# Performance work log

Measured on AMD Instinct MI355X. Metric: run time of the kernel, lower is better.

## Reference

```python
import jax, jax.numpy as jnp
import numpy as np

B, DIM, HEADS, HD, H, W = 1, 256, 8, 32, 64, 64
MLP = int(DIM * 4.0)
EPS = 1e-5


def _ln(x, g, b):
    # LayerNorm over channel dim of NCHW (torch applies it on NHWC last dim)
    mu = x.mean(axis=1, keepdims=True)
    var = ((x - mu) ** 2).mean(axis=1, keepdims=True)
    return (x - mu) / jnp.sqrt(var + EPS) * g[None, :, None, None] + b[None, :, None, None]


def _c1(x, w, b):
    # 1x1 conv: w is [out, in]
    return jnp.einsum('bchw,oc->bohw', x, w) + b[None, :, None, None]


def _c3(x, w, b):
    y = jax.lax.conv_general_dilated(x, w, (1, 1), ((1, 1), (1, 1)),
                                     dimension_numbers=('NCHW', 'OIHW', 'NCHW'))
    return y + b[None, :, None, None]


def setup_inputs() -> dict:
    key = jax.random.key(0)
    ks = jax.random.split(key, 16)
    init = lambda k, s: jax.random.normal(k, s, jnp.float32) * 0.02
    d = {}
    d['rgb_feat'] = jax.random.normal(ks[0], (B, DIM, H, W), jnp.float32)
    d['dpt_feat'] = jax.random.normal(ks[1], (B, DIM, H, W), jnp.float32)
    d['x_dpt'] = jax.random.normal(ks[2], (B, 1, 1024, 1024), jnp.float32)
    d['wq'] = init(ks[3], (DIM, DIM)); d['bq'] = jnp.zeros((DIM,), jnp.float32)
    d['wk'] = init(ks[4], (DIM, DIM)); d['bk'] = jnp.zeros((DIM,), jnp.float32)
    d['wv'] = init(ks[5], (DIM, DIM)); d['bv'] = jnp.zeros((DIM,), jnp.float32)
    d['wo'] = init(ks[6], (DIM, DIM)); d['bo'] = jnp.zeros((DIM,), jnp.float32)
    d['g_rgb'] = jnp.ones((DIM,), jnp.float32); d['b_rgb'] = jnp.zeros((DIM,), jnp.float32)
    d['g_dpt'] = jnp.ones((DIM,), jnp.float32); d['b_dpt'] = jnp.zeros((DIM,), jnp.float32)
    d['g1'] = jnp.ones((DIM,), jnp.float32); d['b1'] = jnp.zeros((DIM,), jnp.float32)
    d['g2'] = jnp.ones((DIM,), jnp.float32); d['b2'] = jnp.zeros((DIM,), jnp.float32)
    d['w_mlp1'] = init(ks[7], (MLP, DIM)); d['b_mlp1'] = jnp.zeros((MLP,), jnp.float32)
    d['w_mlp2'] = init(ks[8], (DIM, MLP)); d['b_mlp2'] = jnp.zeros((DIM,), jnp.float32)
    d['w_de1'] = init(ks[9], (DIM, 1, 3, 3)); d['b_de1'] = jnp.zeros((DIM,), jnp.float32)
    d['w_de2'] = init(ks[10], (DIM, DIM)); d['b_de2'] = jnp.zeros((DIM,), jnp.float32)
    d['pos_emb'] = init(ks[11], (1, DIM, 1, 1))
    d['scale'] = jnp.sqrt(jnp.float32(HD))
    return d


def reference(rgb_feat, dpt_feat, x_dpt, wq, bq, wk, bk, wv, bv, wo, bo,
              g_rgb, b_rgb, g_dpt, b_dpt, g1, b1, g2, b2,
              w_mlp1, b_mlp1, w_mlp2, b_mlp2, w_de1, b_de1, w_de2, b_de2,
              pos_emb, scale):
    Bn, C, Hh, Ww = rgb_feat.shape
    n = Hh * Ww
    rgb_ln = _ln(rgb_feat, g_rgb, b_rgb)
    dpt_ln = _ln(dpt_feat, g_dpt, b_dpt)
    # depth positional embedding: bilinear downsample (align_corners=False) + conv3x3 + relu + conv1x1
    xd = jax.image.resize(x_dpt, (Bn, 1, Hh, Ww), method='bilinear', antialias=False)
    pe = _c1(jax.nn.relu(_c3(xd, w_de1, b_de1)), w_de2, b_de2)
    rgb_ln = rgb_ln + pos_emb + pe
    dpt_ln = dpt_ln + pos_emb + pe
    # QKV as [B, heads, head_dim, N]
    q = _c1(rgb_ln, wq, bq).reshape(Bn, HEADS, HD, n)
    k = _c1(dpt_ln, wk, bk).reshape(Bn, HEADS, HD, n)
    v = _c1(dpt_ln, wv, bv).reshape(Bn, HEADS, HD, n)
    scores = jnp.einsum('bhdn,bhdm->bhnm', q, k) / scale
    attn = jax.nn.softmax(scores, axis=-1)  # dropout is identity in eval
    fused = jnp.einsum('bhnm,bhdm->bhdn', attn, v).reshape(Bn, C, Hh, Ww)
    out = _c1(fused, wo, bo) + rgb_feat
    out_ln = _ln(out, g1, b1)
    h = jax.nn.gelu(_c1(out_ln, w_mlp1, b_mlp1), approximate=False)
    mlp_out = _c1(h, w_mlp2, b_mlp2)
    out2 = mlp_out + out_ln
    return _ln(out2, g2, b2)
```

## Files before the change

### kernel.cpp

```cpp
#include <hip/hip_runtime.h>
#include <hip/hip_bf16.h>
#include <math.h>

constexpr int NTOK = 4096;
constexpr int CDIM = 256;
constexpr int MLPD = 1024;
constexpr int SPLIT = 4;
constexpr float EPS_LN = 1e-5f;

typedef __attribute__((ext_vector_type(8))) short bf16x8;
typedef __attribute__((ext_vector_type(4))) float floatx4;
typedef __attribute__((ext_vector_type(16))) float f32x16;
typedef unsigned short u16;
typedef unsigned int u32;

__device__ __forceinline__ u16 f2bf(float x) {
    union { float f; u32 u; } v; v.f = x;
    u32 r = v.u + 0x7fff + ((v.u >> 16) & 1);
    return (u16)(r >> 16);
}
__device__ __forceinline__ float bf2f(u16 u) {
    union { u32 i; float f; } v; v.i = ((u32)u) << 16; return v.f;
}
__device__ __forceinline__ u32 pkbf(float a, float b) {
    __hip_bfloat162 h = __float22bfloat162_rn(make_float2(a, b));
    union { __hip_bfloat162 h; u32 u; } v; v.h = h; return v.u;
}
__device__ __forceinline__ float gelu_exact(float x) {
    return 0.5f * x * (1.0f + erff(x * 0.70710678118654752f));
}

__global__ __launch_bounds__(256) void k_prep(const float* __restrict__ rgb,
                                              float* __restrict__ rgbT,
                                              const float* __restrict__ dpt,
                                              float* __restrict__ dptT,
                                              const float* __restrict__ xdpt,
                                              const float* __restrict__ w3,
                                              const float* __restrict__ b3,
                                              u16* __restrict__ y,
                                              const float* __restrict__ wq,
                                              const float* __restrict__ wk,
                                              const float* __restrict__ wv,
                                              const float* __restrict__ wo,
                                              const float* __restrict__ wde2,
                                              const float* __restrict__ wm1,
                                              const float* __restrict__ wm2,
                                              u16* __restrict__ arena) {
    int blk = blockIdx.x;
    int t = threadIdx.x;
    if (blk < 512) {
        const float* in = (blk < 256) ? rgb : dpt;
        float* out = (blk < 256) ? rgbT : dptT;
        int tb = blk & 255;
        int c0 = (tb & 63) * 64, r0 = (tb >> 6) * 64;
        __shared__ float T[64][65];
        int rr = t >> 4, cc = (t & 15) * 4;
#pragma unroll
        for (int i = 0; i < 4; ++i) {
            int row = i * 16 + rr;
            float4 v = *(const float4*)(in + (size_t)(r0 + row) * NTOK + c0 + cc);
            T[row][cc] = v.x; T[row][cc + 1] = v.y; T[row][cc + 2] = v.z; T[row][cc + 3] = v.w;
        }
        __syncthreads();
#pragma unroll
        for (int i = 0; i < 4; ++i) {
            int a = i * 16 + rr;
            float4 v;
            v.x = T[cc][a]; v.y = T[cc + 1][a]; v.z = T[cc + 2][a]; v.w = T[cc + 3][a];
            *(float4*)(out + (size_t)(c0 + a) * CDIM + r0 + cc) = v;
        }
    } else if (blk < 768) {
        __shared__ float nb[3][18];
        int n0 = (blk - 512) * 16;
        int yy = n0 >> 6, x0 = n0 & 63;
        if (t < 54) {
            int r = t / 18, cc = t % 18;
            int sy = yy - 1 + r, sx = x0 - 1 + cc;
            float v = 0.f;
            if (sy >= 0 && sy < 64 && sx >= 0 && sx < 64) {
                int r0 = 16 * sy + 7, c0 = 16 * sx + 7;
                v = 0.25f * (xdpt[r0 * 1024 + c0] + xdpt[r0 * 1024 + c0 + 1] +
                             xdpt[(r0 + 1) * 1024 + c0] + xdpt[(r0 + 1) * 1024 + c0 + 1]);
            }
            nb[r][cc] = v;
        }
        __syncthreads();
        float wv9[9];
#pragma unroll
        for (int i = 0; i < 9; ++i) wv9[i] = w3[t * 9 + i];
        float bb = b3[t];
#pragma unroll
        for (int k = 0; k < 16; ++k) {
            float acc = bb;
#pragma unroll
            for (int r = 0; r < 3; ++r)
#pragma unroll
                for (int kx = 0; kx < 3; ++kx) acc += wv9[r * 3 + kx] * nb[r][k + kx];
            y[(size_t)(n0 + k) * CDIM + t] = f2bf(fmaxf(acc, 0.f));
        }
    } else {
        int e0 = (blk - 768) * 1024 + t * 4;
        const float* src; int off;
        if (e0 < 65536)       { src = wq;   off = 0; }
        else if (e0 < 131072) { src = wk;   off = 65536; }
        else if (e0 < 196608) { src = wv;   off = 131072; }
        else if (e0 < 262144) { src = wo;   off = 196608; }
        else if (e0 < 327680) { src = wde2; off = 262144; }
        else if (e0 < 589824) { src = wm1;  off = 327680; }
        else                  { src = wm2;  off = 589824; }
        float4 v = *(const float4*)(src + (e0 - off));
        uint2 o; o.x = pkbf(v.x, v.y); o.y = pkbf(v.z, v.w);
        *(uint2*)(arena + e0) = o;
    }
}

__global__ __launch_bounds__(256) void k_lnT(const void* __restrict__ xA,
                                             const float* __restrict__ gA,
                                             const float* __restrict__ bA,
                                             void* __restrict__ yA,
                                             const void* __restrict__ xB,
                                             const float* __restrict__ gB,
                                             const float* __restrict__ bB,
                                             void* __restrict__ yB,
                                             const u16* __restrict__ pe,
                                             const float* __restrict__ pos,
                                             int xf32) {
    const void* x; const float* g; const float* bb; void* y;
    if (blockIdx.y == 0) { x = xA; g = gA; bb = bA; y = yA; }
    else                 { x = xB; g = gB; bb = bB; y = yB; }
    int n = blockIdx.x * 4 + (threadIdx.x >> 6);
    int lane = threadIdx.x & 63;
    int c = lane * 4;
    float4 xv;
    if (xf32) {
        xv = *((const float4*)x + (size_t)n * 64 + lane);
    } else {
        ushort4 u = *((const ushort4*)x + (size_t)n * 64 + lane);
        xv = make_float4(bf2f(u.x), bf2f(u.y), bf2f(u.z), bf2f(u.w));
    }
    float s = xv.x + xv.y + xv.z + xv.w;
    float s2 = xv.x * xv.x + xv.y * xv.y + xv.z * xv.z + xv.w * xv.w;
#pragma unroll
    for (int off = 1; off < 64; off <<= 1) {
        s += __shfl_xor(s, off, 64);
        s2 += __shfl_xor(s2, off, 64);
    }
    float mu = s * (1.0f / 256.0f);
    float var = s2 * (1.0f / 256.0f) - mu * mu;
    float rsd = rsqrtf(var + EPS_LN);
    float4 g4 = *(const float4*)(g + c);
    float4 b4 = *(const float4*)(bb + c);
    float4 o;
    o.x = (xv.x - mu) * rsd * g4.x + b4.x;
    o.y = (xv.y - mu) * rsd * g4.y + b4.y;
    o.z = (xv.z - mu) * rsd * g4.z + b4.z;
    o.w = (xv.w - mu) * rsd * g4.w + b4.w;
    if (pe) {
        float4 p4 = *(const float4*)(pos + c);
        ushort4 pu = *((const ushort4*)pe + (size_t)n * 64 + lane);
        o.x += p4.x + bf2f(pu.x);
        o.y += p4.y + bf2f(pu.y);
        o.z += p4.z + bf2f(pu.z);
        o.w += p4.w + bf2f(pu.w);
    }
    ushort4 ou;
    ou.x = f2bf(o.x); ou.y = f2bf(o.y); ou.z = f2bf(o.z); ou.w = f2bf(o.w);
    *((ushort4*)y + (size_t)n * 64 + lane) = ou;
}

#define LDB 72
__global__ __launch_bounds__(512) void k_bmm(const u16* __restrict__ X0, const void* __restrict__ W0,
                                             const float* __restrict__ B0, void* __restrict__ Y0, int f0,
                                             const u16* __restrict__ X1, const void* __restrict__ W1,
                                             const float* __restrict__ B1, void* __restrict__ Y1, int f1,
                                             const u16* __restrict__ X2, const void* __restrict__ W2,
                                             const float* __restrict__ B2, void* __restrict__ Y2, int f2,
                                             const void* __restrict__ res, const float* __restrict__ scl,
                                             int M, int K) {
    const u16* X; const void* Wp; const float* bias; void* Yp; int flags;
    if (blockIdx.z == 0)      { X = X0; Wp = W0; bias = B0; Yp = Y0; flags = f0; }
    else if (blockIdx.z == 1) { X = X1; Wp = W1; bias = B1; Yp = Y1; flags = f1; }
    else                      { X = X2; Wp = W2; bias = B2; Yp = Y2; flags = f2; }
    __shared__ u16 Xs[2][64 * LDB];
    __shared__ u16 Ws[2][64 * LDB];
    float* Cred = (float*)&Xs[0][0];

    int tid = threadIdx.x;
    int kg = tid >> 8;
    int t = tid & 255;
    int wid = t >> 6, lane = t & 63;
    int lo16 = lane & 15, quad = lane >> 4;
    int wy = wid & 1, wx = wid >> 1;
    int n0 = blockIdx.x * 64, m0 = blockIdx.y * 64;
    int srow = t >> 2, sseg = t & 3;
    int Khalf = K >> 1;
    int kbase = kg * Khalf;

    floatx4 acc[2][2];
#pragma unroll
    for (int i = 0; i < 2; ++i)
#pragma unroll
        for (int j = 0; j < 2; ++j) acc[i][j] = floatx4{0.f, 0.f, 0.f, 0.f};

    for (int k0 = 0; k0 < Khalf; k0 += 64) {
        int kk = kbase + k0;
        const u16* xp = X + (size_t)(n0 + srow) * K + kk + sseg * 16;
        uint4 xr0 = *(const uint4*)xp;
        uint4 xr1 = *(const uint4*)(xp + 8);
        uint4 wb0, wb1;
        if (flags & 32) {
            const u16* wp = (const u16*)Wp + (size_t)(m0 + srow) * K + kk + sseg * 16;
            wb0 = *(const uint4*)wp;
            wb1 = *(const uint4*)(wp + 8);
        } else {
            const float* wp = (const float*)Wp + (size_t)(m0 + srow) * K + kk + sseg * 16;
            float4 w0 = *(const float4*)wp;
            float4 w1 = *(const float4*)(wp + 4);
            float4 w2 = *(const float4*)(wp + 8);
            float4 w3 = *(const float4*)(wp + 12);
            wb0.x = pkbf(w0.x, w0.y); wb0.y = pkbf(w0.z, w0.w);
            wb0.z = pkbf(w1.x, w1.y); wb0.w = pkbf(w1.z, w1.w);
            wb1.x = pkbf(w2.x, w2.y); wb1.y = pkbf(w2.z, w2.w);
            wb1.z = pkbf(w3.x, w3.y); wb1.w = pkbf(w3.z, w3.w);
        }
        __syncthreads();
        *(uint4*)&Xs[kg][srow * LDB + sseg * 16] = xr0;
        *(uint4*)&Xs[kg][srow * LDB + sseg * 16 + 8] = xr1;
        *(uint4*)&Ws[kg][srow * LDB + sseg * 16] = wb0;
        *(uint4*)&Ws[kg][srow * LDB + sseg * 16 + 8] = wb1;
        __syncthreads();

        const u16* As = (flags & 2) ? &Ws[kg][0] : &Xs[kg][0];
        const u16* Bs = (flags & 2) ? &Xs[kg][0] : &Ws[kg][0];
#pragma unroll
        for (int h = 0; h < 2; ++h) {
            int ko = h * 32 + quad * 8;
            bf16x8 a0 = *(const bf16x8*)&As[(wy * 32 + lo16) * LDB + ko];
            bf16x8 a1 = *(const bf16x8*)&As[(wy * 32 + 16 + lo16) * LDB + ko];
            bf16x8 b0 = *(const bf16x8*)&Bs[(wx * 32 + lo16) * LDB + ko];
            bf16x8 b1 = *(const bf16x8*)&Bs[(wx * 32 + 16 + lo16) * LDB + ko];
            acc[0][0] = __builtin_amdgcn_mfma_f32_16x16x32_bf16(a0, b0, acc[0][0], 0, 0, 0);
            acc[0][1] = __builtin_amdgcn_mfma_f32_16x16x32_bf16(a0, b1, acc[0][1], 0, 0, 0);
            acc[1][0] = __builtin_amdgcn_mfma_f32_16x16x32_bf16(a1, b0, acc[1][0], 0, 0, 0);
            acc[1][1] = __builtin_amdgcn_mfma_f32_16x16x32_bf16(a1, b1, acc[1][1], 0, 0, 0);
        }
    }

    __syncthreads();
    if (kg == 1) {
        float* c = &Cred[t * 17];
#pragma unroll
        for (int i = 0; i < 2; ++i)
#pragma unroll
            for (int j = 0; j < 2; ++j)
#pragma unroll
                for (int r = 0; r < 4; ++r) c[(i * 2 + j) * 4 + r] = acc[i][j][r];
    }
    __syncthreads();
    if (kg == 1) return;
    {
        const float* c = &Cred[t * 17];
#pragma unroll
        for (int i = 0; i < 2; ++i)
#pragma unroll
            for (int j = 0; j < 2; ++j)
#pragma unroll
                for (int r = 0; r < 4; ++r) acc[i][j][r] += c[(i * 2 + j) * 4 + r];
    }

    u16* Y = (u16*)Yp;
    if (flags & 2) {
#pragma unroll
        for (int i = 0; i < 2; ++i)
#pragma unroll
            for (int r = 0; r < 4; ++r) {
                int ch = m0 + wy * 32 + i * 16 + quad * 4 + r;
                float bb = bias[ch];
#pragma unroll
                for (int j = 0; j < 2; ++j) {
                    int tok = n0 + wx * 32 + j * 16 + lo16;
                    Y[(size_t)ch * NTOK + tok] = f2bf(acc[i][j][r] + bb);
                }
            }
    } else {
        float smul = (flags & 16) ? 1.4426950408889634f / scl[0] : 1.0f;
        float bj0 = bias[m0 + wx * 32 + lo16];
        float bj1 = bias[m0 + wx * 32 + 16 + lo16];
        const float* rf = (const float*)res;
        const u16* rb = (const u16*)res;
#pragma unroll
        for (int i = 0; i < 2; ++i)
#pragma unroll
            for (int j = 0; j < 2; ++j) {
                int ch = m0 + wx * 32 + j * 16 + lo16;
                float bb = j ? bj1 : bj0;
#pragma unroll
                for (int r = 0; r < 4; ++r) {
                    int tok = n0 + wy * 32 + i * 16 + quad * 4 + r;
                    float v = (acc[i][j][r] + bb) * smul;
                    if (flags & 1) v = gelu_exact(v);
                    if (flags & 4) v += rf[(size_t)tok * M + ch];
                    if (flags & 8) v += bf2f(rb[(size_t)tok * M + ch]);
                    if (flags & 64)
                        Y[((size_t)(ch >> 5) * NTOK + tok) * 32 + (ch & 31)] = f2bf(v);
                    else
                        Y[(size_t)tok * M + ch] = f2bf(v);
                }
            }
    }
}

#define LDK 40
#define LDV 72
__global__ __launch_bounds__(256) void k_fattn(const u16* __restrict__ Qh,
                                               const u16* __restrict__ Kh,
                                               const u16* __restrict__ Vc,
                                               u16* __restrict__ Op,
                                               float* __restrict__ Lp) {
    __shared__ u16 Kt[64 * LDK];
    __shared__ u16 Vt[32 * LDV];

    int h = blockIdx.y;
    int q0 = blockIdx.x * 128;
    int sp = blockIdx.z;
    int tid = threadIdx.x;
    int wid = tid >> 6, lane = tid & 63;
    int ql = lane & 31, hi = lane >> 5;
    int qtok = q0 + wid * 32 + ql;

    bf16x8 bq0 = *(const bf16x8*)(Qh + ((size_t)h * NTOK + qtok) * 32 + hi * 8);
    bf16x8 bq1 = *(const bf16x8*)(Qh + ((size_t)h * NTOK + qtok) * 32 + 16 + hi * 8);

    int krow = tid >> 2, kseg = tid & 3;
    int vrow = tid >> 3, vseg = tid & 7;
    int kbase = sp * (NTOK / SPLIT);
    const int NITER = NTOK / SPLIT / 64;

    f32x16 oacc = {0.f, 0.f, 0.f, 0.f, 0.f, 0.f, 0.f, 0.f,
                   0.f, 0.f, 0.f, 0.f, 0.f, 0.f, 0.f, 0.f};
    float l = 0.f;

    uint4 kreg = *(const uint4*)(Kh + ((size_t)h * NTOK + kbase + krow) * 32 + kseg * 8);
    uint4 vreg = *(const uint4*)(Vc + (size_t)(h * 32 + vrow) * NTOK + kbase + vseg * 8);

    for (int kt = 0; kt < NITER; ++kt) {
        __syncthreads();
        *(uint4*)&Kt[krow * LDK + kseg * 8] = kreg;
        *(uint4*)&Vt[vrow * LDV + vseg * 8] = vreg;
        __syncthreads();
        if (kt + 1 < NITER) {
            int kn = kbase + (kt + 1) * 64;
            kreg = *(const uint4*)(Kh + ((size_t)h * NTOK + kn + krow) * 32 + kseg * 8);
            vreg = *(const uint4*)(Vc + (size_t)(h * 32 + vrow) * NTOK + kn + vseg * 8);
        }

#pragma unroll
        for (int sub = 0; sub < 2; ++sub) {
            f32x16 s = {0.f, 0.f, 0.f, 0.f, 0.f, 0.f, 0.f, 0.f,
                        0.f, 0.f, 0.f, 0.f, 0.f, 0.f, 0.f, 0.f};
            bf16x8 ak0 = *(const bf16x8*)&Kt[(sub * 32 + ql) * LDK + hi * 8];
            bf16x8 ak1 = *(const bf16x8*)&Kt[(sub * 32 + ql) * LDK + 16 + hi * 8];
            s = __builtin_amdgcn_mfma_f32_32x32x16_bf16(ak0, bq0, s, 0, 0, 0);
            s = __builtin_amdgcn_mfma_f32_32x32x16_bf16(ak1, bq1, s, 0, 0, 0);
            u32 u[8], px[8];
#pragma unroll
            for (int t = 0; t < 8; ++t) {
                float pa = __builtin_amdgcn_exp2f(s[2 * t]);
                float pb = __builtin_amdgcn_exp2f(s[2 * t + 1]);
                l += pa + pb;
                u[t] = pkbf(pa, pb);
            }
#pragma unroll
            for (int t = 0; t < 8; ++t) px[t] = (u32)__shfl_xor((int)u[t], 32, 64);
            uint4 wa, wb;
            wa.x = hi ? px[2] : u[0];
            wa.y = hi ? px[3] : u[1];
            wa.z = hi ? u[2] : px[0];
            wa.w = hi ? u[3] : px[1];
            wb.x = hi ? px[6] : u[4];
            wb.y = hi ? px[7] : u[5];
            wb.z = hi ? u[6] : px[4];
            wb.w = hi ? u[7] : px[5];
            union { uint4 q; bf16x8 v; } pa0, pa1;
            pa0.q = wa; pa1.q = wb;
            bf16x8 bv0 = *(const bf16x8*)&Vt[ql * LDV + sub * 32 + hi * 8];
            bf16x8 bv1 = *(const bf16x8*)&Vt[ql * LDV + sub * 32 + 16 + hi * 8];
            oacc = __builtin_amdgcn_mfma_f32_32x32x16_bf16(pa0.v, bv0, oacc, 0, 0, 0);
            oacc = __builtin_amdgcn_mfma_f32_32x32x16_bf16(pa1.v, bv1, oacc, 0, 0, 0);
        }
    }

    l += __shfl_xor(l, 32, 64);

    size_t obase = ((size_t)(sp * 8 + h) * NTOK + q0 + wid * 32) * 32 + ql;
#pragma unroll
    for (int r = 0; r < 16; ++r) {
        int qrow = (r & 3) + 8 * (r >> 2) + 4 * hi;
        Op[obase + (size_t)qrow * 32] = f2bf(oacc[r]);
    }
    if (hi == 0) Lp[(size_t)(sp * 8 + h) * NTOK + qtok] = l;
}

__global__ __launch_bounds__(256) void k_comb(const u16* __restrict__ Op,
                                              const float* __restrict__ Lp,
                                              u16* __restrict__ fused) {
    int n = blockIdx.x * 4 + (threadIdx.x >> 6);
    int lane = threadIdx.x & 63;
    int c = lane * 4;
    int h = c >> 5, d = c & 31;
    float4 o = {0.f, 0.f, 0.f, 0.f};
    float l = 0.f;
#pragma unroll
    for (int s = 0; s < SPLIT; ++s) {
        size_t base = ((size_t)(s * 8 + h) * NTOK + n) * 32 + d;
        uint2 u = *(const uint2*)(Op + base);
        o.x += bf2f((u16)(u.x & 0xffff)); o.y += bf2f((u16)(u.x >> 16));
        o.z += bf2f((u16)(u.y & 0xffff)); o.w += bf2f((u16)(u.y >> 16));
        l += Lp[(size_t)(s * 8 + h) * NTOK + n];
    }
    float inv = 1.0f / l;
    uint2 w;
    w.x = pkbf(o.x * inv, o.y * inv);
    w.y = pkbf(o.z * inv, o.w * inv);
    *(uint2*)(fused + (size_t)n * CDIM + c) = w;
}

__global__ __launch_bounds__(256) void k_lntr(const u16* __restrict__ x,
                                              const float* __restrict__ g,
                                              const float* __restrict__ b,
                                              float* __restrict__ out) {
    __shared__ float T[16][260];
    int n0 = blockIdx.x * 16;
    int t = threadIdx.x;
    int tk = t >> 4, seg = t & 15;
    float v[16];
    {
        const u16* p = x + (size_t)(n0 + tk) * CDIM + seg * 16;
        uint4 a = *(const uint4*)p;
        uint4 bq = *(const uint4*)(p + 8);
        u32 uu[8] = {a.x, a.y, a.z, a.w, bq.x, bq.y, bq.z, bq.w};
#pragma unroll
        for (int i = 0; i < 8; ++i) {
            v[2 * i] = bf2f((u16)(uu[i] & 0xffff));
            v[2 * i + 1] = bf2f((u16)(uu[i] >> 16));
        }
    }
    float s = 0.f, s2 = 0.f;
#pragma unroll
    for (int i = 0; i < 16; ++i) { s += v[i]; s2 += v[i] * v[i]; }
#pragma unroll
    for (int off = 1; off < 16; off <<= 1) {
        s += __shfl_xor(s, off, 64);
        s2 += __shfl_xor(s2, off, 64);
    }
    float mu = s * (1.0f / 256.0f);
    float var = s2 * (1.0f / 256.0f) - mu * mu;
    float rsd = rsqrtf(var + EPS_LN);
#pragma unroll
    for (int i = 0; i < 16; ++i) {
        int c = seg * 16 + i;
        T[tk][c] = (v[i] - mu) * rsd * g[c] + b[c];
    }
    __syncthreads();
    int c = t;
    float o[16];
#pragma unroll
    for (int j = 0; j < 16; ++j) o[j] = T[j][c];
    float* dst = out + (size_t)c * NTOK + n0;
#pragma unroll
    for (int j = 0; j < 4; ++j) {
        float4 w = {o[4 * j], o[4 * j + 1], o[4 * j + 2], o[4 * j + 3]};
        *(float4*)(dst + 4 * j) = w;
    }
}

extern "C" void kernel_launch(void* const* d_in, const int* in_sizes, int n_in,
                              void* d_out, int out_size, void* d_ws, size_t ws_size,
                              hipStream_t stream) {
    const float* rgb    = (const float*)d_in[0];
    const float* dpt    = (const float*)d_in[1];
    const float* x_dpt  = (const float*)d_in[2];
    const float* wq     = (const float*)d_in[3];
    const float* bq     = (const float*)d_in[4];
    const float* wk     = (const float*)d_in[5];
    const float* bk     = (const float*)d_in[6];
    const float* wv     = (const float*)d_in[7];
    const float* bv     = (const float*)d_in[8];
    const float* wo     = (const float*)d_in[9];
    const float* bo     = (const float*)d_in[10];
    const float* g_rgb  = (const float*)d_in[11];
    const float* b_rgb  = (const float*)d_in[12];
    const float* g_dpt  = (const float*)d_in[13];
    const float* b_dpt  = (const float*)d_in[14];
    const float* g1     = (const float*)d_in[15];
    const float* b1     = (const float*)d_in[16];
    const float* g2     = (const float*)d_in[17];
    const float* b2     = (const float*)d_in[18];
    const float* w_mlp1 = (const float*)d_in[19];
    const float* b_mlp1 = (const float*)d_in[20];
    const float* w_mlp2 = (const float*)d_in[21];
    const float* b_mlp2 = (const float*)d_in[22];
    const float* w_de1  = (const float*)d_in[23];
    const float* b_de1  = (const float*)d_in[24];
    const float* w_de2  = (const float*)d_in[25];
    const float* b_de2  = (const float*)d_in[26];
    const float* pos    = (const float*)d_in[27];
    const float* scale  = (const float*)d_in[28];
    float* out = (float*)d_out;

    char* base = (char*)d_ws;
    const size_t MB = 1u << 20;
    float* rgbT    = (float*)(base + 0 * MB);
    float* dptT    = (float*)(base + 4 * MB);
    u16*   outT    = (u16*)(base + 4 * MB);
    float* Lp      = (float*)(base + 6 * MB);
    u16*   out_lnT = (u16*)(base + 6 * MB);
    u16*   relu3T  = (u16*)(base + 8 * MB);
    u16*   Op      = (u16*)(base + 8 * MB);
    u16*   hT      = (u16*)(base + 8 * MB);
    u16*   peT     = (u16*)(base + 10 * MB);
    u16*   aqT     = (u16*)(base + 12 * MB);
    u16*   akvT    = (u16*)(base + 14 * MB);
    u16*   Qhm     = (u16*)(base + 16 * MB);
    u16*   out2T   = (u16*)(base + 16 * MB);
    u16*   Khm     = (u16*)(base + 18 * MB);
    u16*   Vcm     = (u16*)(base + 20 * MB);
    u16*   fusedT  = (u16*)(base + 22 * MB);
    u16*   arena   = (u16*)(base + 24 * MB);

    bool aw = ws_size >= 26 * MB;
    int wf = aw ? 32 : 0;
    const void* Wq  = aw ? (const void*)(arena + 0)      : (const void*)wq;
    const void* Wk  = aw ? (const void*)(arena + 65536)  : (const void*)wk;
    const void* Wv  = aw ? (const void*)(arena + 131072) : (const void*)wv;
    const void* Wo  = aw ? (const void*)(arena + 196608) : (const void*)wo;
    const void* Wd2 = aw ? (const void*)(arena + 262144) : (const void*)w_de2;
    const void* Wm1 = aw ? (const void*)(arena + 327680) : (const void*)w_mlp1;
    const void* Wm2 = aw ? (const void*)(arena + 589824) : (const void*)w_mlp2;

    k_prep<<<aw ? 512 + 256 + 832 : 512 + 256, 256, 0, stream>>>(
        rgb, rgbT, dpt, dptT, x_dpt, w_de1, b_de1, relu3T,
        wq, wk, wv, wo, w_de2, w_mlp1, w_mlp2, arena);
    k_bmm<<<dim3(64, 4, 1), 512, 0, stream>>>(relu3T, Wd2, b_de2, peT, wf,
                                              nullptr, nullptr, nullptr, nullptr, 0,
                                              nullptr, nullptr, nullptr, nullptr, 0,
                                              nullptr, nullptr, CDIM, CDIM);
    k_lnT<<<dim3(1024, 2), 256, 0, stream>>>(rgbT, g_rgb, b_rgb, aqT,
                                             dptT, g_dpt, b_dpt, akvT,
                                             peT, pos, 1);
    k_bmm<<<dim3(64, 4, 3), 512, 0, stream>>>(aqT, Wq, bq, Qhm, wf | 16 | 64,
                                              akvT, Wk, bk, Khm, wf | 64,
                                              akvT, Wv, bv, Vcm, wf | 2,
                                              nullptr, scale, CDIM, CDIM);
    k_fattn<<<dim3(32, 8, SPLIT), 256, 0, stream>>>(Qhm, Khm, Vcm, Op, Lp);
    k_comb<<<1024, 256, 0, stream>>>(Op, Lp, fusedT);
    k_bmm<<<dim3(64, 4, 1), 512, 0, stream>>>(fusedT, Wo, bo, outT, wf | 4,
                                              nullptr, nullptr, nullptr, nullptr, 0,
                                              nullptr, nullptr, nullptr, nullptr, 0,
                                              rgbT, nullptr, CDIM, CDIM);
    k_lnT<<<dim3(1024, 1), 256, 0, stream>>>(outT, g1, b1, out_lnT,
                                             nullptr, nullptr, nullptr, nullptr,
                                             nullptr, nullptr, 0);
    k_bmm<<<dim3(64, 16, 1), 512, 0, stream>>>(out_lnT, Wm1, b_mlp1, hT, wf | 1,
                                               nullptr, nullptr, nullptr, nullptr, 0,
                                               nullptr, nullptr, nullptr, nullptr, 0,
                                               nullptr, nullptr, MLPD, CDIM);
    k_bmm<<<dim3(64, 4, 1), 512, 0, stream>>>(hT, Wm2, b_mlp2, out2T, wf | 8,
                                              nullptr, nullptr, nullptr, nullptr, 0,
                                              nullptr, nullptr, nullptr, nullptr, 0,
                                              out_lnT, nullptr, CDIM, MLPD);
    k_lntr<<<256, 256, 0, stream>>>(out2T, g2, b2, out);
}
```

Baseline: 215.7 us.

## Double-buffer attention K/V tiles and raise split-K to eight when workspace allows

The flash-attention kernel now keeps two LDS buffers for the K and V tiles. This lets one barrier per iteration replace two. The host also picks a key-split factor of 8 instead of 4 when the workspace is at least 68 MB, placing the partial outputs in a higher workspace region. This doubles the attention grid for more parallelism and latency hiding, at the cost of more partial-output traffic and a larger combine step.

```diff
diff --git a/kernel.cpp b/kernel.cpp
--- a/kernel.cpp
+++ b/kernel.cpp
@@ -5,7 +5,6 @@
 constexpr int NTOK = 4096;
 constexpr int CDIM = 256;
 constexpr int MLPD = 1024;
-constexpr int SPLIT = 4;
 constexpr float EPS_LN = 1e-5f;
 
 typedef __attribute__((ext_vector_type(8))) short bf16x8;
@@ -316,9 +315,10 @@
                                                const u16* __restrict__ Kh,
                                                const u16* __restrict__ Vc,
                                                u16* __restrict__ Op,
-                                               float* __restrict__ Lp) {
-    __shared__ u16 Kt[64 * LDK];
-    __shared__ u16 Vt[32 * LDV];
+                                               float* __restrict__ Lp,
+                                               int niter) {
+    __shared__ u16 Kt[2][64 * LDK];
+    __shared__ u16 Vt[2][32 * LDV];
 
     int h = blockIdx.y;
     int q0 = blockIdx.x * 128;
@@ -328,13 +328,13 @@
     int ql = lane & 31, hi = lane >> 5;
     int qtok = q0 + wid * 32 + ql;
 
-    bf16x8 bq0 = *(const bf16x8*)(Qh + ((size_t)h * NTOK + qtok) * 32 + hi * 8);
-    bf16x8 bq1 = *(const bf16x8*)(Qh + ((size_t)h * NTOK + qtok) * 32 + 16 + hi * 8);
+    const u16* qp = Qh + ((size_t)h * NTOK + qtok) * 32 + hi * 8;
+    bf16x8 bq0 = *(const bf16x8*)(qp);
+    bf16x8 bq1 = *(const bf16x8*)(qp + 16);
 
     int krow = tid >> 2, kseg = tid & 3;
     int vrow = tid >> 3, vseg = tid & 7;
-    int kbase = sp * (NTOK / SPLIT);
-    const int NITER = NTOK / SPLIT / 64;
+    int kbase = sp * (niter * 64);
 
     f32x16 oacc = {0.f, 0.f, 0.f, 0.f, 0.f, 0.f, 0.f, 0.f,
                    0.f, 0.f, 0.f, 0.f, 0.f, 0.f, 0.f, 0.f};
@@ -343,12 +343,12 @@
     uint4 kreg = *(const uint4*)(Kh + ((size_t)h * NTOK + kbase + krow) * 32 + kseg * 8);
     uint4 vreg = *(const uint4*)(Vc + (size_t)(h * 32 + vrow) * NTOK + kbase + vseg * 8);
 
-    for (int kt = 0; kt < NITER; ++kt) {
+    for (int kt = 0; kt < niter; ++kt) {
+        int cb = kt & 1;
+        *(uint4*)&Kt[cb][krow * LDK + kseg * 8] = kreg;
+        *(uint4*)&Vt[cb][vrow * LDV + vseg * 8] = vreg;
         __syncthreads();
-        *(uint4*)&Kt[krow * LDK + kseg * 8] = kreg;
-        *(uint4*)&Vt[vrow * LDV + vseg * 8] = vreg;
-        __syncthreads();
-        if (kt + 1 < NITER) {
+        if (kt + 1 < niter) {
             int kn = kbase + (kt + 1) * 64;
             kreg = *(const uint4*)(Kh + ((size_t)h * NTOK + kn + krow) * 32 + kseg * 8);
             vreg = *(const uint4*)(Vc + (size_t)(h * 32 + vrow) * NTOK + kn + vseg * 8);
@@ -358,8 +358,8 @@
         for (int sub = 0; sub < 2; ++sub) {
             f32x16 s = {0.f, 0.f, 0.f, 0.f, 0.f, 0.f, 0.f, 0.f,
                         0.f, 0.f, 0.f, 0.f, 0.f, 0.f, 0.f, 0.f};
-            bf16x8 ak0 = *(const bf16x8*)&Kt[(sub * 32 + ql) * LDK + hi * 8];
-            bf16x8 ak1 = *(const bf16x8*)&Kt[(sub * 32 + ql) * LDK + 16 + hi * 8];
+            bf16x8 ak0 = *(const bf16x8*)&Kt[cb][(sub * 32 + ql) * LDK + hi * 8];
+            bf16x8 ak1 = *(const bf16x8*)&Kt[cb][(sub * 32 + ql) * LDK + 16 + hi * 8];
             s = __builtin_amdgcn_mfma_f32_32x32x16_bf16(ak0, bq0, s, 0, 0, 0);
             s = __builtin_amdgcn_mfma_f32_32x32x16_bf16(ak1, bq1, s, 0, 0, 0);
             u32 u[8], px[8];
@@ -383,8 +383,8 @@
             wb.w = hi ? u[7] : px[5];
             union { uint4 q; bf16x8 v; } pa0, pa1;
             pa0.q = wa; pa1.q = wb;
-            bf16x8 bv0 = *(const bf16x8*)&Vt[ql * LDV + sub * 32 + hi * 8];
-            bf16x8 bv1 = *(const bf16x8*)&Vt[ql * LDV + sub * 32 + 16 + hi * 8];
+            bf16x8 bv0 = *(const bf16x8*)&Vt[cb][ql * LDV + sub * 32 + hi * 8];
+            bf16x8 bv1 = *(const bf16x8*)&Vt[cb][ql * LDV + sub * 32 + 16 + hi * 8];
             oacc = __builtin_amdgcn_mfma_f32_32x32x16_bf16(pa0.v, bv0, oacc, 0, 0, 0);
             oacc = __builtin_amdgcn_mfma_f32_32x32x16_bf16(pa1.v, bv1, oacc, 0, 0, 0);
         }
@@ -403,15 +403,15 @@
 
 __global__ __launch_bounds__(256) void k_comb(const u16* __restrict__ Op,
                                               const float* __restrict__ Lp,
-                                              u16* __restrict__ fused) {
+                                              u16* __restrict__ fused,
+                                              int split) {
     int n = blockIdx.x * 4 + (threadIdx.x >> 6);
     int lane = threadIdx.x & 63;
     int c = lane * 4;
     int h = c >> 5, d = c & 31;
     float4 o = {0.f, 0.f, 0.f, 0.f};
     float l = 0.f;
-#pragma unroll
-    for (int s = 0; s < SPLIT; ++s) {
+    for (int s = 0; s < split; ++s) {
         size_t base = ((size_t)(s * 8 + h) * NTOK + n) * 32 + d;
         uint2 u = *(const uint2*)(Op + base);
         o.x += bf2f((u16)(u.x & 0xffff)); o.y += bf2f((u16)(u.x >> 16));
@@ -513,10 +513,10 @@
     float* rgbT    = (float*)(base + 0 * MB);
     float* dptT    = (float*)(base + 4 * MB);
     u16*   outT    = (u16*)(base + 4 * MB);
-    float* Lp      = (float*)(base + 6 * MB);
+    float* Lp4     = (float*)(base + 6 * MB);
     u16*   out_lnT = (u16*)(base + 6 * MB);
     u16*   relu3T  = (u16*)(base + 8 * MB);
-    u16*   Op      = (u16*)(base + 8 * MB);
+    u16*   Op4     = (u16*)(base + 8 * MB);
     u16*   hT      = (u16*)(base + 8 * MB);
     u16*   peT     = (u16*)(base + 10 * MB);
     u16*   aqT     = (u16*)(base + 12 * MB);
@@ -537,6 +537,10 @@
     const void* Wd2 = aw ? (const void*)(arena + 262144) : (const void*)w_de2;
     const void* Wm1 = aw ? (const void*)(arena + 327680) : (const void*)w_mlp1;
     const void* Wm2 = aw ? (const void*)(arena + 589824) : (const void*)w_mlp2;
+
+    int split = (ws_size >= 68 * MB) ? 8 : 4;
+    u16*   Op = (split == 8) ? (u16*)(base + 32 * MB) : Op4;
+    float* Lp = (split == 8) ? (float*)(base + 48 * MB) : Lp4;
 
     k_prep<<<aw ? 512 + 256 + 832 : 512 + 256, 256, 0, stream>>>(
         rgb, rgbT, dpt, dptT, x_dpt, w_de1, b_de1, relu3T,
@@ -552,8 +556,9 @@
                                               akvT, Wk, bk, Khm, wf | 64,
                                               akvT, Wv, bv, Vcm, wf | 2,
                                               nullptr, scale, CDIM, CDIM);
-    k_fattn<<<dim3(32, 8, SPLIT), 256, 0, stream>>>(Qhm, Khm, Vcm, Op, Lp);
-    k_comb<<<1024, 256, 0, stream>>>(Op, Lp, fusedT);
+    k_fattn<<<dim3(32, 8, split), 256, 0, stream>>>(Qhm, Khm, Vcm, Op, Lp,
+                                                    NTOK / split / 64);
+    k_comb<<<1024, 256, 0, stream>>>(Op, Lp, fusedT, split);
     k_bmm<<<dim3(64, 4, 1), 512, 0, stream>>>(fusedT, Wo, bo, outT, wf | 4,
                                               nullptr, nullptr, nullptr, nullptr, 0,
                                               nullptr, nullptr, nullptr, nullptr, 0,
```

Result: no change. 212.7 us (-1.4%).
